# Kernel optimization log

Measured on AMD Instinct MI355X. Metric: run time of the kernel, lower is better.

Reference implementation:

```python
import jax, jax.numpy as jnp
import numpy as np

N, DIM = 100000, 512
HID = DIM // 2


def _mlp(z, W1, b1, W2, b2):
    # shared scorer: [N, dim] -> [N, 1]
    h = jax.nn.relu(z @ W1 + b1)
    return h @ W2 + b2


def setup_inputs() -> dict:
    key = jax.random.key(0)
    k1, k2, k3, k4 = jax.random.split(key, 4)
    s1 = 1.0 / np.sqrt(DIM)
    s2 = 1.0 / np.sqrt(HID)
    return {
        "z1": jax.random.normal(k1, (N, DIM), dtype=jnp.float32),
        "z2": jax.random.normal(k2, (N, DIM), dtype=jnp.float32),
        "W1": jax.random.normal(k3, (DIM, HID), dtype=jnp.float32) * s1,
        "b1": jnp.zeros((HID,), dtype=jnp.float32),
        "W2": jax.random.normal(k4, (HID, 1), dtype=jnp.float32) * s2,
        "b2": jnp.zeros((1,), dtype=jnp.float32),
    }


def reference(z1, z2, W1, b1, W2, b2):
    x = _mlp(z1, W1, b1, W2, b2)  # [N, 1]
    y = _mlp(z2, W1, b1, W2, b2)  # [N, 1]
    # exp-normalize pair: score_x = e^x / (e^x + e^y) == sigmoid(x - y)
    # computed exactly as in the original (plain exp, no max-subtract)
    e_x = jnp.exp(x)
    e_y = jnp.exp(y)
    denom = e_x + e_y
    score_x = e_x / denom  # [N, 1]
    score_y = e_y / denom  # [N, 1]
    # diag(score) @ z  ==  score * z  (row-wise broadcast scale)
    return score_x * z1 + score_y * z2
```

## Files before the change

### kernel.cpp

```cpp
#include <hip/hip_runtime.h>
#include <hip/hip_bf16.h>
#include <cmath>

#define DIM 512
#define HID 256
#define ROWS_PB 16
#define NCHUNK 16

typedef __attribute__((ext_vector_type(8))) short short8;
typedef __attribute__((ext_vector_type(4))) float f32x4;

__device__ __forceinline__ unsigned short f2bf(float f) {
  union { float f; unsigned u; } v; v.f = f;
  unsigned u = v.u;
  return (unsigned short)((u + 0x7FFFu + ((u >> 16) & 1u)) >> 16);
}
__device__ __forceinline__ float bf2f(short h) {
  union { unsigned u; float f; } v;
  v.u = ((unsigned)(unsigned short)h) << 16;
  return v.f;
}

__global__ void w1_swz_kernel(const float* __restrict__ W1,
                              unsigned short* __restrict__ w1s) {
  int tid = blockIdx.x * blockDim.x + threadIdx.x;
  if (tid >= DIM * HID) return;
  int k = tid / HID;
  int c = tid - k * HID;
  w1s[(((k >> 3) * HID) + c) * 8 + (k & 7)] = f2bf(W1[tid]);
}

__device__ __forceinline__ short8 cvt8(const f32x4 p0, const f32x4 p1) {
  short8 r;
  r[0] = (short)f2bf(p0[0]); r[1] = (short)f2bf(p0[1]);
  r[2] = (short)f2bf(p0[2]); r[3] = (short)f2bf(p0[3]);
  r[4] = (short)f2bf(p1[0]); r[5] = (short)f2bf(p1[1]);
  r[6] = (short)f2bf(p1[2]); r[7] = (short)f2bf(p1[3]);
  return r;
}

__device__ __forceinline__ void wcombine(float wa, const short8 a, float wb,
                                         const short8 b, f32x4& o0, f32x4& o1) {
#pragma unroll
  for (int i = 0; i < 4; ++i) {
    o0[i] = wa * bf2f(a[i]) + wb * bf2f(b[i]);
    o1[i] = wa * bf2f(a[i + 4]) + wb * bf2f(b[i + 4]);
  }
}

__global__ __launch_bounds__(256, 2) void fa_main_kernel(
    const float* __restrict__ z1, const float* __restrict__ z2,
    const unsigned short* __restrict__ w1s,
    const float* __restrict__ bias1, const float* __restrict__ W2,
    const float* __restrict__ bias2, float* __restrict__ out, int n) {
  __shared__ short8 Az[2 * NCHUNK * 64];
  __shared__ float xs2[2][2][ROWS_PB];

  const int t = threadIdx.x;
  const int w = t >> 6;
  const int l = t & 63;
  const int l15 = l & 15, l16 = l >> 4;
  const int s = w & 1;
  const int h = w >> 1;
  const int row0 = blockIdx.x * ROWS_PB;
  const int myrow = row0 + l15;
  const bool rok = myrow < n;
  const float* zz = s ? z2 : z1;
  const float* ap = zz + (size_t)myrow * DIM + (l16 << 3);
  const f32x4 zf4 = (f32x4){0.f, 0.f, 0.f, 0.f};

  {
    f32x4 pp[8][2];
#pragma unroll
    for (int j = 0; j < 8; ++j) {
      const float* p = ap + ((h * 8 + j) << 5);
      pp[j][0] = rok ? *(const f32x4*)(p) : zf4;
      pp[j][1] = rok ? *(const f32x4*)(p + 4) : zf4;
    }
#pragma unroll
    for (int j = 0; j < 8; ++j)
      Az[(s * NCHUNK + h * 8 + j) * 64 + l] = cvt8(pp[j][0], pp[j][1]);
  }
  __syncthreads();

  short8 af[NCHUNK];
#pragma unroll
  for (int c = 0; c < NCHUNK; ++c) af[c] = Az[(s * NCHUNK + c) * 64 + l];

  f32x4 acc[8];
#pragma unroll
  for (int f = 0; f < 8; ++f) acc[f] = zf4;

  const short8* gB = (const short8*)w1s;
  const int bbase = (l16 << 8) + (h << 7) + l15;
  short8 b0[8], b1[8];
#pragma unroll
  for (int f = 0; f < 8; ++f) b0[f] = gB[bbase + (f << 4)];
#pragma unroll
  for (int cc = 0; cc < NCHUNK / 2; ++cc) {
    const int c0 = 2 * cc, c1 = 2 * cc + 1;
#pragma unroll
    for (int f = 0; f < 8; ++f) b1[f] = gB[(c1 << 10) + bbase + (f << 4)];
#pragma unroll
    for (int f = 0; f < 8; ++f)
      acc[f] = __builtin_amdgcn_mfma_f32_16x16x32_bf16(af[c0], b0[f], acc[f],
                                                       0, 0, 0);
    if (c1 + 1 < NCHUNK) {
#pragma unroll
      for (int f = 0; f < 8; ++f)
        b0[f] = gB[((c1 + 1) << 10) + bbase + (f << 4)];
    }
#pragma unroll
    for (int f = 0; f < 8; ++f)
      acc[f] = __builtin_amdgcn_mfma_f32_16x16x32_bf16(af[c1], b1[f], acc[f],
                                                       0, 0, 0);
  }

  float part[4] = {0.f, 0.f, 0.f, 0.f};
#pragma unroll
  for (int f = 0; f < 8; ++f) {
    const int cc = (h << 7) + (f << 4) + l15;
    const float w2v = W2[cc];
    const float b1v = bias1[cc];
#pragma unroll
    for (int r = 0; r < 4; ++r) {
      const float hh = acc[f][r] + b1v;
      part[r] += (hh > 0.f) ? hh * w2v : 0.f;
    }
  }
#pragma unroll
  for (int r = 0; r < 4; ++r) {
#pragma unroll
    for (int m = 1; m < 16; m <<= 1) part[r] += __shfl_xor(part[r], m, 16);
  }
  if (l15 == 0) {
#pragma unroll
    for (int r = 0; r < 4; ++r) xs2[s][h][(l16 << 2) + r] = part[r];
  }
  __syncthreads();

  const float x = xs2[0][0][l15] + xs2[0][1][l15];
  const float y = xs2[1][0][l15] + xs2[1][1][l15];
  const float d = y - x;
  const float sx = 1.f / (1.f + __expf(d));
  const float sy = 1.f - sx;
  float* orow = out + (size_t)myrow * DIM + (l16 << 3);
  if (rok) {
#pragma unroll
    for (int j = 0; j < 4; ++j) {
      const int c = (w << 2) + j;
      const short8 a0 = Az[(0 * NCHUNK + c) * 64 + l];
      const short8 a1 = Az[(1 * NCHUNK + c) * 64 + l];
      f32x4 o0, o1;
      wcombine(sx, a0, sy, a1, o0, o1);
      *(f32x4*)(orow + (c << 5)) = o0;
      *(f32x4*)(orow + (c << 5) + 4) = o1;
    }
  }
}

extern "C" void kernel_launch(void* const* d_in, const int* in_sizes, int n_in,
                              void* d_out, int out_size, void* d_ws,
                              size_t ws_size, hipStream_t stream) {
  const float* z1 = (const float*)d_in[0];
  const float* z2 = (const float*)d_in[1];
  const float* W1 = (const float*)d_in[2];
  const float* b1 = (const float*)d_in[3];
  const float* W2 = (const float*)d_in[4];
  const float* b2 = (const float*)d_in[5];
  float* out = (float*)d_out;
  const int n = in_sizes[0] / DIM;
  unsigned short* w1s = (unsigned short*)d_ws;

  hipLaunchKernelGGL(w1_swz_kernel, dim3((DIM * HID + 255) / 256), dim3(256),
                     0, stream, W1, w1s);
  const int nwg = (n + ROWS_PB - 1) / ROWS_PB;
  hipLaunchKernelGGL(fa_main_kernel, dim3(nwg), dim3(256), 0, stream, z1, z2,
                     w1s, b1, W2, b2, out, n);
}
```

Measured before the change: 215.6 us.

## Stage W1 chunks cooperatively through double-buffered LDS instead of per-wave global loads

Each block now loads each 16KB chunk of the swizzled bf16 W1 once, cooperatively across all 256 threads, into a double-buffered shared-memory tile. Waves then read their B fragments from LDS. Before, each wave fetched its own fragments directly from global memory. This cuts redundant global/L2 traffic for the weights (4 waves shared overlapping data). The cost is an extra 32KB of LDS per block, which may lower occupancy, plus a __syncthreads per chunk.

```diff
diff --git a/kernel.cpp b/kernel.cpp
--- a/kernel.cpp
+++ b/kernel.cpp
@@ -6,9 +6,11 @@
 #define HID 256
 #define ROWS_PB 16
 #define NCHUNK 16
+#define CB 16384
 
 typedef __attribute__((ext_vector_type(8))) short short8;
 typedef __attribute__((ext_vector_type(4))) float f32x4;
+typedef __attribute__((ext_vector_type(4))) unsigned int u32x4;
 
 __device__ __forceinline__ unsigned short f2bf(float f) {
   union { float f; unsigned u; } v; v.f = f;
@@ -54,6 +56,7 @@
     const float* __restrict__ bias1, const float* __restrict__ W2,
     const float* __restrict__ bias2, float* __restrict__ out, int n) {
   __shared__ short8 Az[2 * NCHUNK * 64];
+  __shared__ char Bbuf[2][CB];
   __shared__ float xs2[2][2][ROWS_PB];
 
   const int t = threadIdx.x;
@@ -69,6 +72,26 @@
   const float* ap = zz + (size_t)myrow * DIM + (l16 << 3);
   const f32x4 zf4 = (f32x4){0.f, 0.f, 0.f, 0.f};
 
+  u32x4 breg0, breg1, breg2, breg3;
+#define BLOAD(c)                                            \
+  {                                                         \
+    const u32x4* g = (const u32x4*)w1s + (c) * 1024 + t;    \
+    breg0 = g[0];                                           \
+    breg1 = g[256];                                         \
+    breg2 = g[512];                                         \
+    breg3 = g[768];                                         \
+  }
+#define BWRITE(c)                                           \
+  {                                                         \
+    u32x4* d = (u32x4*)&Bbuf[(c) & 1][0] + t;               \
+    d[0] = breg0;                                           \
+    d[256] = breg1;                                         \
+    d[512] = breg2;                                         \
+    d[768] = breg3;                                         \
+  }
+
+  BLOAD(0);
+  __builtin_amdgcn_sched_barrier(0);
   {
     f32x4 pp[8][2];
 #pragma unroll
@@ -77,6 +100,7 @@
       pp[j][0] = rok ? *(const f32x4*)(p) : zf4;
       pp[j][1] = rok ? *(const f32x4*)(p + 4) : zf4;
     }
+    BWRITE(0);
 #pragma unroll
     for (int j = 0; j < 8; ++j)
       Az[(s * NCHUNK + h * 8 + j) * 64 + l] = cvt8(pp[j][0], pp[j][1]);
@@ -91,29 +115,20 @@
 #pragma unroll
   for (int f = 0; f < 8; ++f) acc[f] = zf4;
 
-  const short8* gB = (const short8*)w1s;
-  const int bbase = (l16 << 8) + (h << 7) + l15;
-  short8 b0[8], b1[8];
 #pragma unroll
-  for (int f = 0; f < 8; ++f) b0[f] = gB[bbase + (f << 4)];
+  for (int c = 0; c < NCHUNK; ++c) {
+    if (c + 1 < NCHUNK) BLOAD(c + 1);
+    __builtin_amdgcn_sched_barrier(0);
+    const short8* bp =
+        (const short8*)&Bbuf[c & 1][0] + (l16 << 8) + (h << 7) + l15;
 #pragma unroll
-  for (int cc = 0; cc < NCHUNK / 2; ++cc) {
-    const int c0 = 2 * cc, c1 = 2 * cc + 1;
-#pragma unroll
-    for (int f = 0; f < 8; ++f) b1[f] = gB[(c1 << 10) + bbase + (f << 4)];
-#pragma unroll
-    for (int f = 0; f < 8; ++f)
-      acc[f] = __builtin_amdgcn_mfma_f32_16x16x32_bf16(af[c0], b0[f], acc[f],
-                                                       0, 0, 0);
-    if (c1 + 1 < NCHUNK) {
-#pragma unroll
-      for (int f = 0; f < 8; ++f)
-        b0[f] = gB[((c1 + 1) << 10) + bbase + (f << 4)];
+    for (int f = 0; f < 8; ++f) {
+      const short8 bf = bp[f << 4];
+      acc[f] =
+          __builtin_amdgcn_mfma_f32_16x16x32_bf16(af[c], bf, acc[f], 0, 0, 0);
     }
-#pragma unroll
-    for (int f = 0; f < 8; ++f)
-      acc[f] = __builtin_amdgcn_mfma_f32_16x16x32_bf16(af[c1], b1[f], acc[f],
-                                                       0, 0, 0);
+    if (c + 1 < NCHUNK) BWRITE(c + 1);
+    __syncthreads();
   }
 
   float part[4] = {0.f, 0.f, 0.f, 0.f};
@@ -157,6 +172,8 @@
       *(f32x4*)(orow + (c << 5) + 4) = o1;
     }
   }
+#undef BLOAD
+#undef BWRITE
 }
 
 extern "C" void kernel_launch(void* const* d_in, const int* in_sizes, int n_in,
```

After: 206.7 us. 1.04x faster.
